# Optimization experiments

Measured on AMD Instinct MI355X. Metric: run time of the kernel, lower is better.

Reference implementation:

```python
import math
import jax, jax.numpy as jnp
import numpy as np

H = 16          # num_attention_heads
DH = 64         # attention_head_size
D = H * DH      # hidden_size
MAX_POS = 1024  # max_position_embeddings


def setup_inputs() -> dict:
    key = jax.random.key(0)
    ks = jax.random.split(key, 9)
    B, S = 8, 1024
    scale = 0.02
    return {
        "hidden_states": jax.random.normal(ks[0], (B, S, D), dtype=jnp.float32),
        "attention_mask": jnp.zeros((B, 1, 1, S), dtype=jnp.float32),
        "Wq": jax.random.normal(ks[1], (D, D), dtype=jnp.float32) * scale,
        "bq": jnp.zeros((D,), dtype=jnp.float32),
        "Wk": jax.random.normal(ks[2], (D, D), dtype=jnp.float32) * scale,
        "bk": jnp.zeros((D,), dtype=jnp.float32),
        "Wv": jax.random.normal(ks[3], (D, D), dtype=jnp.float32) * scale,
        "bv": jnp.zeros((D,), dtype=jnp.float32),
        "dist_emb": jax.random.normal(ks[4], (2 * MAX_POS - 1, DH), dtype=jnp.float32) * scale,
    }


def reference(hidden_states, attention_mask, Wq, bq, Wk, bk, Wv, bv, dist_emb):
    B, S, _ = hidden_states.shape
    # projections -> [B, H, S, DH]
    def heads(x):
        return x.reshape(B, S, H, DH).transpose(0, 2, 1, 3)
    q = heads(hidden_states @ Wq + bq)
    k = heads(hidden_states @ Wk + bk)
    v = heads(hidden_states @ Wv + bv)

    # fp32_cast_query_key == 'manual': cast q,k to fp32 before matmul (already fp32 here)
    scores = jnp.einsum("bhld,bhrd->bhlr", q.astype(jnp.float32), k.astype(jnp.float32))
    scores = scores / math.sqrt(DH)

    # relative_key_query positional bias
    pos = jnp.arange(S)
    distance = pos[:, None] - pos[None, :] + (MAX_POS - 1)   # [S, S]
    pe = dist_emb[distance].astype(q.dtype)                   # [S, S, DH]
    scores = scores + jnp.einsum("bhld,lrd->bhlr", q, pe) \
                     + jnp.einsum("bhrd,lrd->bhlr", k, pe)

    scores = scores + attention_mask
    # fp32_cast_attention_scores=True: softmax in fp32
    probs = jax.nn.softmax(scores.astype(jnp.float32), axis=-1).astype(hidden_states.dtype)

    ctx = jnp.einsum("bhlr,bhrd->bhld", probs, v)  # [B, H, S, DH]
    ctx = ctx.transpose(0, 2, 1, 3).reshape(B, S, D)
    return ctx
```

## Files before the change

kernel.cpp:

```cpp
#include <hip/hip_runtime.h>
#include <stdint.h>

typedef unsigned short u16;
typedef short bf16x8 __attribute__((ext_vector_type(8)));
typedef float f32x4 __attribute__((ext_vector_type(4)));
typedef u16 u16x8 __attribute__((ext_vector_type(8)));
typedef u16 u16x4 __attribute__((ext_vector_type(4)));

#define NB 8
#define NS 1024
#define NH 16
#define NDH 64
#define ND 1024

__device__ __forceinline__ u16 f2b(float x){
  unsigned u = __float_as_uint(x);
  u += 0x7FFFu + ((u >> 16) & 1u);
  return (u16)(u >> 16);
}
__device__ __forceinline__ float b2f(u16 h){ return __uint_as_float(((unsigned)h) << 16); }

__global__ void cast_f32_bf16(const float* __restrict__ in, u16* __restrict__ out, long n){
  long i = ((long)blockIdx.x * blockDim.x + threadIdx.x) * 8;
  if (i + 8 <= n){
    float4 a = *(const float4*)&in[i];
    float4 b = *(const float4*)&in[i + 4];
    u16x8 o;
    o[0]=f2b(a.x); o[1]=f2b(a.y); o[2]=f2b(a.z); o[3]=f2b(a.w);
    o[4]=f2b(b.x); o[5]=f2b(b.y); o[6]=f2b(b.z); o[7]=f2b(b.w);
    *(u16x8*)&out[i] = o;
  }
}

__global__ void transpose_w(const float* __restrict__ Wq, const float* __restrict__ Wk,
                            const float* __restrict__ Wv, u16* __restrict__ wt){
  __shared__ float tile[64][65];
  int p = blockIdx.z;
  const float* W = (p == 0) ? Wq : ((p == 1) ? Wk : Wv);
  int n0 = blockIdx.x * 64, k0 = blockIdx.y * 64;
  int t = threadIdx.x;
  int row = t >> 2, cb = (t & 3) * 16;
  #pragma unroll
  for (int cc = 0; cc < 4; ++cc){
    float4 v = *(const float4*)&W[(size_t)(k0 + row) * ND + n0 + cb + cc * 4];
    tile[row][cb + cc*4 + 0] = v.x; tile[row][cb + cc*4 + 1] = v.y;
    tile[row][cb + cc*4 + 2] = v.z; tile[row][cb + cc*4 + 3] = v.w;
  }
  __syncthreads();
  u16x8 o0, o1;
  #pragma unroll
  for (int kk = 0; kk < 8; ++kk) o0[kk] = f2b(tile[cb + kk][row]);
  #pragma unroll
  for (int kk = 0; kk < 8; ++kk) o1[kk] = f2b(tile[cb + 8 + kk][row]);
  size_t ob = ((size_t)(p * ND + n0 + row)) * ND + k0 + cb;
  *(u16x8*)&wt[ob]     = o0;
  *(u16x8*)&wt[ob + 8] = o1;
}

__global__ __launch_bounds__(256) void qkv_gemm(
    const u16* __restrict__ hsb, const u16* __restrict__ wtb,
    const float* __restrict__ bq, const float* __restrict__ bk, const float* __restrict__ bv,
    u16* __restrict__ qb, u16* __restrict__ kb, u16* __restrict__ vt){
  __shared__ __attribute__((aligned(16))) u16 Al[128 * 32];
  __shared__ __attribute__((aligned(16))) u16 Bl[128 * 32];
  int t = threadIdx.x;
  int lane = t & 63, w = t >> 6;
  int li = lane & 15, g = lane >> 4;
  int m0 = blockIdx.y * 128, n0 = blockIdx.x * 128;
  int wm = (w >> 1) * 64, wn = (w & 1) * 64;
  f32x4 acc[4][4];
  #pragma unroll
  for (int a = 0; a < 4; ++a)
    #pragma unroll
    for (int b = 0; b < 4; ++b){ f32x4 z = {0.f,0.f,0.f,0.f}; acc[a][b] = z; }

  for (int kt = 0; kt < 32; ++kt){
    __syncthreads();
    #pragma unroll
    for (int ph = 0; ph < 2; ++ph){
      int c = ph * 256 + t;
      int row = c >> 2, ch = c & 3;
      const u16* ga = &hsb[(size_t)(m0 + row) * ND + kt * 32 + ch * 8];
      __builtin_amdgcn_global_load_lds((const __attribute__((address_space(1))) void*)ga,
          (__attribute__((address_space(3))) void*)&Al[(ph * 256 + w * 64) * 8], 16, 0, 0);
      const u16* gb = &wtb[(size_t)(n0 + row) * ND + kt * 32 + ch * 8];
      __builtin_amdgcn_global_load_lds((const __attribute__((address_space(1))) void*)gb,
          (__attribute__((address_space(3))) void*)&Bl[(ph * 256 + w * 64) * 8], 16, 0, 0);
    }
    asm volatile("s_waitcnt vmcnt(0)" ::: "memory");
    __syncthreads();
    bf16x8 af[4], bfr[4];
    #pragma unroll
    for (int mt = 0; mt < 4; ++mt)
      af[mt] = *(const bf16x8*)&Al[(wm + mt * 16 + li) * 32 + g * 8];
    #pragma unroll
    for (int nt = 0; nt < 4; ++nt)
      bfr[nt] = *(const bf16x8*)&Bl[(wn + nt * 16 + li) * 32 + g * 8];
    #pragma unroll
    for (int mt = 0; mt < 4; ++mt)
      #pragma unroll
      for (int nt = 0; nt < 4; ++nt)
        acc[mt][nt] = __builtin_amdgcn_mfma_f32_16x16x32_bf16(af[mt], bfr[nt], acc[mt][nt], 0, 0, 0);
  }

  int proj = n0 >> 10;
  const float* bias = (proj == 0) ? bq : ((proj == 1) ? bk : bv);
  #pragma unroll
  for (int nt = 0; nt < 4; ++nt){
    int n = n0 + wn + nt * 16 + li;
    int nc = n & 1023;
    float bv_ = bias[nc];
    #pragma unroll
    for (int mt = 0; mt < 4; ++mt){
      #pragma unroll
      for (int r = 0; r < 4; ++r){
        int m = m0 + wm + mt * 16 + g * 4 + r;
        u16 hv = f2b(acc[mt][nt][r] + bv_);
        if (proj == 0)      qb[(size_t)m * ND + nc] = hv;
        else if (proj == 1) kb[(size_t)m * ND + nc] = hv;
        else {
          int bb = m >> 10, s = m & 1023;
          int hh = nc >> 6, dh = nc & 63;
          vt[((size_t)(bb * NH + hh) * NDH + dh) * NS + s] = hv;
        }
      }
    }
  }
}

__global__ __launch_bounds__(256) void attn(
    const u16* __restrict__ qb, const u16* __restrict__ kb,
    const u16* __restrict__ vt, const u16* __restrict__ eb,
    const float* __restrict__ mask, float* __restrict__ out){
  __shared__ __attribute__((aligned(16))) u16 k_lds[64 * 72];
  __shared__ __attribute__((aligned(16))) u16 v_lds[64 * 72];
  __shared__ __attribute__((aligned(16))) u16 e_lds[128 * 72];
  __shared__ __attribute__((aligned(16))) u16 u2_lds[128 * 72];
  __shared__ __attribute__((aligned(16))) u16 w2_lds[128 * 72];
  int t = threadIdx.x, lane = t & 63, w = t >> 6;
  int li = lane & 15, g = lane >> 4;
  int lt = blockIdx.x, bh = blockIdx.y;
  int b = bh >> 4, h = bh & 15;
  int l0 = lt * 64;

  bf16x8 qf[2];
  {
    size_t qoff = ((size_t)(b * NS + l0 + w * 16 + li)) * ND + h * NDH;
    qf[0] = *(const bf16x8*)&qb[qoff + 0 + g * 8];
    qf[1] = *(const bf16x8*)&qb[qoff + 32 + g * 8];
  }
  f32x4 oacc[4];
  #pragma unroll
  for (int i = 0; i < 4; ++i){ f32x4 z = {0.f,0.f,0.f,0.f}; oacc[i] = z; }
  float mold[4] = {-1e30f, -1e30f, -1e30f, -1e30f};
  float lsum[4] = {0.f, 0.f, 0.f, 0.f};

  for (int kt2 = 0; kt2 < 16; ++kt2){
    int r0 = kt2 * 64;
    int ebase = l0 - r0 + 960;
    __syncthreads();
    {
      u16x8 rk[2], rv[2], re[4];
      #pragma unroll
      for (int ph = 0; ph < 2; ++ph){
        int c = ph * 256 + t, row = c >> 3, ch = c & 7;
        rk[ph] = *(const u16x8*)&kb[((size_t)(b * NS + r0 + row)) * ND + h * NDH + ch * 8];
        rv[ph] = *(const u16x8*)&vt[((size_t)(bh * NDH + row)) * NS + r0 + ch * 8];
      }
      #pragma unroll
      for (int ph = 0; ph < 4; ++ph){
        int c = ph * 256 + t, row = c >> 3, ch = c & 7;
        int er = ebase + row; er = er > 2046 ? 2046 : er;
        re[ph] = *(const u16x8*)&eb[(size_t)er * NDH + ch * 8];
      }
      #pragma unroll
      for (int ph = 0; ph < 2; ++ph){
        int c = ph * 256 + t, row = c >> 3, ch = c & 7;
        *(u16x8*)&k_lds[row * 72 + ch * 8] = rk[ph];
        *(u16x8*)&v_lds[row * 72 + ch * 8] = rv[ph];
      }
      #pragma unroll
      for (int ph = 0; ph < 4; ++ph){
        int c = ph * 256 + t, row = c >> 3, ch = c & 7;
        *(u16x8*)&e_lds[row * 72 + ch * 8] = re[ph];
      }
    }
    __syncthreads();

    bf16x8 kf[2];
    kf[0] = *(const bf16x8*)&k_lds[(w * 16 + li) * 72 + 0 + g * 8];
    kf[1] = *(const bf16x8*)&k_lds[(w * 16 + li) * 72 + 32 + g * 8];

    #pragma unroll
    for (int nt = 0; nt < 8; ++nt){
      f32x4 ua = {0.f,0.f,0.f,0.f}, wa = {0.f,0.f,0.f,0.f};
      #pragma unroll
      for (int ks = 0; ks < 2; ++ks){
        bf16x8 ef = *(const bf16x8*)&e_lds[(nt * 16 + li) * 72 + ks * 32 + g * 8];
        ua = __builtin_amdgcn_mfma_f32_16x16x32_bf16(qf[ks], ef, ua, 0, 0, 0);
        wa = __builtin_amdgcn_mfma_f32_16x16x32_bf16(kf[ks], ef, wa, 0, 0, 0);
      }
      u16x4 up, wp;
      #pragma unroll
      for (int r = 0; r < 4; ++r){ up[r] = f2b(ua[r]); wp[r] = f2b(wa[r]); }
      *(u16x4*)&u2_lds[(nt * 16 + li) * 72 + w * 16 + g * 4] = up;
      *(u16x4*)&w2_lds[(nt * 16 + li) * 72 + w * 16 + g * 4] = wp;
    }

    f32x4 sacc[4];
    #pragma unroll
    for (int jt = 0; jt < 4; ++jt){
      f32x4 z = {0.f,0.f,0.f,0.f}; sacc[jt] = z;
      #pragma unroll
      for (int ks = 0; ks < 2; ++ks){
        bf16x8 kbf = *(const bf16x8*)&k_lds[(jt * 16 + li) * 72 + ks * 32 + g * 8];
        sacc[jt] = __builtin_amdgcn_mfma_f32_16x16x32_bf16(qf[ks], kbf, sacc[jt], 0, 0, 0);
      }
    }
    __syncthreads();

    float sv[4][4];
    #pragma unroll
    for (int jt = 0; jt < 4; ++jt){
      int j = jt * 16 + li;
      float mk = mask[b * NS + r0 + j];
      #pragma unroll
      for (int r = 0; r < 4; ++r){
        int ib = w * 16 + g * 4 + r;
        int tt = ib - j + 63;
        float u  = b2f(u2_lds[tt * 72 + ib]);
        float ww = b2f(w2_lds[tt * 72 + j]);
        sv[jt][r] = sacc[jt][r] * 0.125f + u + ww + mk;
      }
    }

    float rmax[4], rsum[4];
    #pragma unroll
    for (int r = 0; r < 4; ++r)
      rmax[r] = fmaxf(fmaxf(sv[0][r], sv[1][r]), fmaxf(sv[2][r], sv[3][r]));
    #pragma unroll
    for (int xm = 1; xm <= 8; xm <<= 1)
      #pragma unroll
      for (int r = 0; r < 4; ++r)
        rmax[r] = fmaxf(rmax[r], __shfl_xor(rmax[r], xm));
    float mnew[4], fac[4];
    #pragma unroll
    for (int r = 0; r < 4; ++r){
      mnew[r] = fmaxf(mold[r], rmax[r]);
      fac[r]  = __expf(mold[r] - mnew[r]);
    }
    float pr[4][4];
    #pragma unroll
    for (int r = 0; r < 4; ++r) rsum[r] = 0.f;
    #pragma unroll
    for (int jt = 0; jt < 4; ++jt)
      #pragma unroll
      for (int r = 0; r < 4; ++r){
        pr[jt][r] = __expf(sv[jt][r] - mnew[r]);
        rsum[r] += pr[jt][r];
      }
    #pragma unroll
    for (int xm = 1; xm <= 8; xm <<= 1)
      #pragma unroll
      for (int r = 0; r < 4; ++r)
        rsum[r] += __shfl_xor(rsum[r], xm);
    #pragma unroll
    for (int r = 0; r < 4; ++r){
      lsum[r] = lsum[r] * fac[r] + rsum[r];
      mold[r] = mnew[r];
    }
    #pragma unroll
    for (int nt2 = 0; nt2 < 4; ++nt2)
      #pragma unroll
      for (int r = 0; r < 4; ++r)
        oacc[nt2][r] *= fac[r];

    __syncthreads();
    u16* p_w = &u2_lds[(w * 16) * 72];
    #pragma unroll
    for (int jt = 0; jt < 4; ++jt)
      #pragma unroll
      for (int r = 0; r < 4; ++r)
        p_w[(g * 4 + r) * 72 + jt * 16 + li] = f2b(pr[jt][r]);

    #pragma unroll
    for (int ks = 0; ks < 2; ++ks){
      bf16x8 pf = *(const bf16x8*)&p_w[li * 72 + ks * 32 + g * 8];
      #pragma unroll
      for (int nt2 = 0; nt2 < 4; ++nt2){
        bf16x8 vf = *(const bf16x8*)&v_lds[(nt2 * 16 + li) * 72 + ks * 32 + g * 8];
        oacc[nt2] = __builtin_amdgcn_mfma_f32_16x16x32_bf16(pf, vf, oacc[nt2], 0, 0, 0);
      }
    }
  }

  #pragma unroll
  for (int nt2 = 0; nt2 < 4; ++nt2)
    #pragma unroll
    for (int r = 0; r < 4; ++r){
      int row = l0 + w * 16 + g * 4 + r;
      out[((size_t)(b * NS + row)) * ND + h * NDH + nt2 * 16 + li] = oacc[nt2][r] / lsum[r];
    }
}

extern "C" void kernel_launch(void* const* d_in, const int* in_sizes, int n_in,
                              void* d_out, int out_size, void* d_ws, size_t ws_size,
                              hipStream_t stream){
  (void)in_sizes; (void)n_in; (void)out_size; (void)ws_size;
  const float* hs   = (const float*)d_in[0];
  const float* mask = (const float*)d_in[1];
  const float* Wq   = (const float*)d_in[2];
  const float* bq   = (const float*)d_in[3];
  const float* Wk   = (const float*)d_in[4];
  const float* bk   = (const float*)d_in[5];
  const float* Wv   = (const float*)d_in[6];
  const float* bv   = (const float*)d_in[7];
  const float* de   = (const float*)d_in[8];
  float* out = (float*)d_out;
  char* ws = (char*)d_ws;

  u16* hsb = (u16*)(ws);
  u16* wtb = (u16*)(ws + 16777216);
  u16* eb  = (u16*)(ws + 23068672);
  u16* qb  = (u16*)(ws + 23330816);
  u16* kb  = (u16*)(ws + 40108032);
  u16* vt  = (u16*)(ws + 56885248);

  cast_f32_bf16<<<4096, 256, 0, stream>>>(hs, hsb, 8388608L);
  cast_f32_bf16<<<64, 256, 0, stream>>>(de, eb, 131008L);
  transpose_w<<<dim3(16, 16, 3), 256, 0, stream>>>(Wq, Wk, Wv, wtb);
  qkv_gemm<<<dim3(24, 64), 256, 0, stream>>>(hsb, wtb, bq, bk, bv, qb, kb, vt);
  attn<<<dim3(16, 128), 256, 0, stream>>>(qb, kb, vt, eb, mask, out);
}
```

Before: 419.7 us.

## Read distance embeddings directly from global and XOR-swizzle bias LDS buffers

Removes the e_lds staging buffer, so the attention kernel loads distance-embedding fragments straight from global memory (L2/L1 cached) inside the MFMA loop. The u2/w2 bias buffers drop their padding and use an XOR-swizzled 128-byte row layout to avoid LDS bank conflicts. The probability scratch reuses the swizzled u2 buffer. Together with the smaller LDS footprint, launch bounds now request 3 blocks per CU to raise occupancy, at the risk of global-load latency on the embedding reads and register pressure.

Measured after the change: 493.9 us. 17.7% more time.

```diff
diff --git a/kernel.cpp b/kernel.cpp
--- a/kernel.cpp
+++ b/kernel.cpp
@@ -12,6 +12,13 @@
 #define NH 16
 #define NDH 64
 #define ND 1024
+
+#define AS1 __attribute__((address_space(1)))
+#define AS3 __attribute__((address_space(3)))
+
+__device__ __forceinline__ int SWZ(int row, int colbyte){
+  return (row << 7) + (colbyte ^ ((row & 7) << 4));
+}
 
 __device__ __forceinline__ u16 f2b(float x){
   unsigned u = __float_as_uint(x);
@@ -81,11 +88,11 @@
       int c = ph * 256 + t;
       int row = c >> 2, ch = c & 3;
       const u16* ga = &hsb[(size_t)(m0 + row) * ND + kt * 32 + ch * 8];
-      __builtin_amdgcn_global_load_lds((const __attribute__((address_space(1))) void*)ga,
-          (__attribute__((address_space(3))) void*)&Al[(ph * 256 + w * 64) * 8], 16, 0, 0);
+      __builtin_amdgcn_global_load_lds((const AS1 void*)ga,
+          (AS3 void*)&Al[(ph * 256 + w * 64) * 8], 16, 0, 0);
       const u16* gb = &wtb[(size_t)(n0 + row) * ND + kt * 32 + ch * 8];
-      __builtin_amdgcn_global_load_lds((const __attribute__((address_space(1))) void*)gb,
-          (__attribute__((address_space(3))) void*)&Bl[(ph * 256 + w * 64) * 8], 16, 0, 0);
+      __builtin_amdgcn_global_load_lds((const AS1 void*)gb,
+          (AS3 void*)&Bl[(ph * 256 + w * 64) * 8], 16, 0, 0);
     }
     asm volatile("s_waitcnt vmcnt(0)" ::: "memory");
     __syncthreads();
@@ -128,20 +135,25 @@
   }
 }
 
-__global__ __launch_bounds__(256) void attn(
+__global__ __launch_bounds__(256, 3) void attn(
     const u16* __restrict__ qb, const u16* __restrict__ kb,
     const u16* __restrict__ vt, const u16* __restrict__ eb,
     const float* __restrict__ mask, float* __restrict__ out){
   __shared__ __attribute__((aligned(16))) u16 k_lds[64 * 72];
   __shared__ __attribute__((aligned(16))) u16 v_lds[64 * 72];
-  __shared__ __attribute__((aligned(16))) u16 e_lds[128 * 72];
-  __shared__ __attribute__((aligned(16))) u16 u2_lds[128 * 72];
-  __shared__ __attribute__((aligned(16))) u16 w2_lds[128 * 72];
+  __shared__ __attribute__((aligned(16))) u16 u2[128 * 64];
+  __shared__ __attribute__((aligned(16))) u16 w2[128 * 64];
+
   int t = threadIdx.x, lane = t & 63, w = t >> 6;
   int li = lane & 15, g = lane >> 4;
   int lt = blockIdx.x, bh = blockIdx.y;
   int b = bh >> 4, h = bh & 15;
   int l0 = lt * 64;
+  int iA  = w * 16 + g * 4;
+  int iA2 = iA * 2;
+  int li2 = li * 2;
+  int ttc = iA + 63 - li;
+  int colw = iA2;
 
   bf16x8 qf[2];
   {
@@ -158,9 +170,10 @@
   for (int kt2 = 0; kt2 < 16; ++kt2){
     int r0 = kt2 * 64;
     int ebase = l0 - r0 + 960;
+
     __syncthreads();
     {
-      u16x8 rk[2], rv[2], re[4];
+      u16x8 rk[2], rv[2];
       #pragma unroll
       for (int ph = 0; ph < 2; ++ph){
         int c = ph * 256 + t, row = c >> 3, ch = c & 7;
@@ -168,22 +181,11 @@
         rv[ph] = *(const u16x8*)&vt[((size_t)(bh * NDH + row)) * NS + r0 + ch * 8];
       }
       #pragma unroll
-      for (int ph = 0; ph < 4; ++ph){
-        int c = ph * 256 + t, row = c >> 3, ch = c & 7;
-        int er = ebase + row; er = er > 2046 ? 2046 : er;
-        re[ph] = *(const u16x8*)&eb[(size_t)er * NDH + ch * 8];
-      }
-      #pragma unroll
       for (int ph = 0; ph < 2; ++ph){
         int c = ph * 256 + t, row = c >> 3, ch = c & 7;
         *(u16x8*)&k_lds[row * 72 + ch * 8] = rk[ph];
         *(u16x8*)&v_lds[row * 72 + ch * 8] = rv[ph];
       }
-      #pragma unroll
-      for (int ph = 0; ph < 4; ++ph){
-        int c = ph * 256 + t, row = c >> 3, ch = c & 7;
-        *(u16x8*)&e_lds[row * 72 + ch * 8] = re[ph];
-      }
     }
     __syncthreads();
 
@@ -193,18 +195,20 @@
 
     #pragma unroll
     for (int nt = 0; nt < 8; ++nt){
+      int trow = nt * 16 + li;
+      int er = ebase + trow; if (er > 2046) er = 2046;
       f32x4 ua = {0.f,0.f,0.f,0.f}, wa = {0.f,0.f,0.f,0.f};
       #pragma unroll
-      for (int ks = 0; ks < 2; ++ks){
-        bf16x8 ef = *(const bf16x8*)&e_lds[(nt * 16 + li) * 72 + ks * 32 + g * 8];
-        ua = __builtin_amdgcn_mfma_f32_16x16x32_bf16(qf[ks], ef, ua, 0, 0, 0);
-        wa = __builtin_amdgcn_mfma_f32_16x16x32_bf16(kf[ks], ef, wa, 0, 0, 0);
+      for (int k2 = 0; k2 < 2; ++k2){
+        bf16x8 ef = *(const bf16x8*)&eb[(size_t)er * NDH + k2 * 32 + g * 8];
+        ua = __builtin_amdgcn_mfma_f32_16x16x32_bf16(qf[k2], ef, ua, 0, 0, 0);
+        wa = __builtin_amdgcn_mfma_f32_16x16x32_bf16(kf[k2], ef, wa, 0, 0, 0);
       }
       u16x4 up, wp;
       #pragma unroll
       for (int r = 0; r < 4; ++r){ up[r] = f2b(ua[r]); wp[r] = f2b(wa[r]); }
-      *(u16x4*)&u2_lds[(nt * 16 + li) * 72 + w * 16 + g * 4] = up;
-      *(u16x4*)&w2_lds[(nt * 16 + li) * 72 + w * 16 + g * 4] = wp;
+      *(u16x4*)((char*)u2 + SWZ(trow, colw)) = up;
+      *(u16x4*)((char*)w2 + SWZ(trow, colw)) = wp;
     }
 
     f32x4 sacc[4];
@@ -212,9 +216,9 @@
     for (int jt = 0; jt < 4; ++jt){
       f32x4 z = {0.f,0.f,0.f,0.f}; sacc[jt] = z;
       #pragma unroll
-      for (int ks = 0; ks < 2; ++ks){
-        bf16x8 kbf = *(const bf16x8*)&k_lds[(jt * 16 + li) * 72 + ks * 32 + g * 8];
-        sacc[jt] = __builtin_amdgcn_mfma_f32_16x16x32_bf16(qf[ks], kbf, sacc[jt], 0, 0, 0);
+      for (int k2 = 0; k2 < 2; ++k2){
+        bf16x8 kbf = *(const bf16x8*)&k_lds[(jt * 16 + li) * 72 + k2 * 32 + g * 8];
+        sacc[jt] = __builtin_amdgcn_mfma_f32_16x16x32_bf16(qf[k2], kbf, sacc[jt], 0, 0, 0);
       }
     }
     __syncthreads();
@@ -222,14 +226,15 @@
     float sv[4][4];
     #pragma unroll
     for (int jt = 0; jt < 4; ++jt){
-      int j = jt * 16 + li;
-      float mk = mask[b * NS + r0 + j];
+      float mk = mask[b * NS + r0 + jt * 16 + li];
+      int j2 = jt * 32 + li2;
       #pragma unroll
       for (int r = 0; r < 4; ++r){
-        int ib = w * 16 + g * 4 + r;
-        int tt = ib - j + 63;
-        float u  = b2f(u2_lds[tt * 72 + ib]);
-        float ww = b2f(w2_lds[tt * 72 + j]);
+        int tt = ttc + r - jt * 16;
+        int byU = (tt << 7) + ((iA2 + 2 * r) ^ ((tt & 7) << 4));
+        int byW = (tt << 7) + (j2 ^ ((tt & 7) << 4));
+        float u  = b2f(*(const u16*)((const char*)u2 + byU));
+        float ww = b2f(*(const u16*)((const char*)w2 + byW));
         sv[jt][r] = sacc[jt][r] * 0.125f + u + ww + mk;
       }
     }
@@ -276,19 +281,20 @@
         oacc[nt2][r] *= fac[r];
 
     __syncthreads();
-    u16* p_w = &u2_lds[(w * 16) * 72];
     #pragma unroll
     for (int jt = 0; jt < 4; ++jt)
       #pragma unroll
-      for (int r = 0; r < 4; ++r)
-        p_w[(g * 4 + r) * 72 + jt * 16 + li] = f2b(pr[jt][r]);
-
-    #pragma unroll
-    for (int ks = 0; ks < 2; ++ks){
-      bf16x8 pf = *(const bf16x8*)&p_w[li * 72 + ks * 32 + g * 8];
+      for (int r = 0; r < 4; ++r){
+        int prow = w * 16 + g * 4 + r;
+        *(u16*)((char*)u2 + SWZ(prow, jt * 32 + li2)) = f2b(pr[jt][r]);
+      }
+
+    #pragma unroll
+    for (int k2 = 0; k2 < 2; ++k2){
+      bf16x8 pf = *(const bf16x8*)((const char*)u2 + SWZ(w * 16 + li, k2 * 64 + g * 16));
       #pragma unroll
       for (int nt2 = 0; nt2 < 4; ++nt2){
-        bf16x8 vf = *(const bf16x8*)&v_lds[(nt2 * 16 + li) * 72 + ks * 32 + g * 8];
+        bf16x8 vf = *(const bf16x8*)&v_lds[(nt2 * 16 + li) * 72 + k2 * 32 + g * 8];
         oacc[nt2] = __builtin_amdgcn_mfma_f32_16x16x32_bf16(pf, vf, oacc[nt2], 0, 0, 0);
       }
     }
```
